# Kernel optimization log

Measured on AMD Instinct MI355X. Metric: run time of the kernel, lower is better.

The kernel has to match this reference:

```python
import jax, jax.numpy as jnp
import numpy as np

SHIFTS = [1, 2, 4]  # matches init_kwargs 'shifts' (all in range 0 < s < channels)


def setup_inputs() -> dict:
    key = jax.random.key(0)
    k1, k2, k3 = jax.random.split(key, 3)
    B, H, L, D = 4, 1, 2048, 512
    factor = 4
    proj_in = 2 * len(SHIFTS) * D  # cli_mode='full' -> 2 components per shift
    x = jax.random.normal(k1, (B, H, L, D), dtype=jnp.float32)
    W = jax.random.normal(k2, (factor, D), dtype=jnp.float32) * 0.05
    # glorot-ish scale for the projection kernel
    proj_kernel = jax.random.normal(k3, (proj_in, D), dtype=jnp.float32) * (1.0 / np.sqrt(proj_in))
    proj_bias = jnp.zeros((D,), dtype=jnp.float32)
    return {"x": x, "W": W, "proj_kernel": proj_kernel, "proj_bias": proj_bias}


def reference(x, W, proj_kernel, proj_bias):
    # x: (B, H, L, D); W: (k, D) slot multivectors
    k, D = W.shape
    B, H, L, _ = x.shape
    # coarse[-1] treated as zeros; non-anchor slots source previous coarse vector
    coarse_prev = jnp.pad(x, ((0, 0), (0, 0), (1, 0), (0, 0)))[:, :, :-1, :]
    # src: (B, H, L, k, D) — slots 0..k-2 from coarse_prev, slot k-1 (anchor) from x
    src = jnp.concatenate(
        [jnp.repeat(coarse_prev[:, :, :, None, :], k - 1, axis=3),
         x[:, :, :, None, :]],
        axis=3,
    )
    W_b = W[None, None, None, :, :]  # (1,1,1,k,D)
    components = []
    for s in SHIFTS:
        src_s = jnp.roll(src, s, axis=-1)
        W_s_b = jnp.roll(W, s, axis=-1)[None, None, None, :, :]
        sw = src * W_s_b
        components.append(sw - W_b * src_s)        # wedge part
        components.append(jax.nn.silu(sw))          # inner part (full mode)
    g = jnp.concatenate(components, axis=-1)  # (B,H,L,k, 2*len(shifts)*D)
    fine = jnp.einsum('bhlkc,cd->bhlkd', g, proj_kernel) + proj_bias
    return fine.reshape(B, H, L * k, D)
```

## Files before the change

### kernel.cpp

```cpp
#include <hip/hip_runtime.h>
#include <cstdint>
#include <cstddef>

#define D_DIM 512
#define L_DIM 2048
#define KB_DIM 2048
#define KS_DIM 1536
#define NROWS_X 2049
#define M_TOT 32768

typedef __bf16 bf16x8 __attribute__((ext_vector_type(8)));
typedef float  f32x4  __attribute__((ext_vector_type(4)));

__device__ __forceinline__ unsigned f2bf(float f) {
  unsigned u = __float_as_uint(f);
  u += 0x7FFF + ((u >> 16) & 1);
  return u >> 16;
}
__device__ __forceinline__ float bf2f(unsigned short u) {
  return __uint_as_float(((unsigned)u) << 16);
}
__device__ __forceinline__ void gld_lds16(const void* g, void* l) {
  __builtin_amdgcn_global_load_lds((const __attribute__((address_space(1))) void*)g,
                                   (__attribute__((address_space(3))) void*)l,
                                   16, 0, 0);
}

__global__ void convert_x(const float* __restrict__ x, unsigned short* __restrict__ XbfZ) {
  const int b = blockIdx.y;
  const int idx = blockIdx.x * 256 + threadIdx.x;
  if (idx >= NROWS_X * 128) return;
  const int rr = idx >> 7;
  const int c4 = idx & 127;
  uint2 p = {0u, 0u};
  if (rr > 0) {
    float4 v = reinterpret_cast<const float4*>(x)[((size_t)b * L_DIM + rr - 1) * 128 + c4];
    p.x = f2bf(v.x) | (f2bf(v.y) << 16);
    p.y = f2bf(v.z) | (f2bf(v.w) << 16);
  }
  reinterpret_cast<uint2*>(XbfZ)[((size_t)b * NROWS_X + rr) * 128 + c4] = p;
}

__global__ void build_B(const float* __restrict__ P, const float* __restrict__ W,
                        unsigned short* __restrict__ Ball,
                        unsigned short* __restrict__ Wtab, int buildWtab) {
  if (buildWtab && blockIdx.x == 0) {
    for (int i = threadIdx.x; i < 6144; i += 256) {
      const int c = i & 511; const int rest = i >> 9;
      const int si = rest % 3; const int jj = rest / 3;
      Wtab[(jj * 3 + si) * 512 + c] =
          (unsigned short)f2bf(W[jj * 512 + ((c - (1 << si)) & 511)]);
    }
  }
  const int bx = blockIdx.x;
  const int j = bx >> 6, dt = (bx >> 3) & 7, ct = bx & 7;
  const int t = threadIdx.x;
  const int d = dt * 64 + (t & 63);
  const int cbase = ct * 64 + (t >> 6) * 16;
  unsigned short bufd[16];
  unsigned short bufs[3][16];
  #pragma unroll
  for (int cc = 0; cc < 16; ++cc) {
    const int c = cbase + cc;
    float qd = 0.f;
    #pragma unroll
    for (int si = 0; si < 3; ++si) {
      const int s = 1 << si;
      const int cm = (c - s) & 511, cp = (c + s) & 511;
      qd += W[j * 512 + cm] * P[((size_t)(2 * si) * 512 + c) * 512 + d]
          - W[j * 512 + cp] * P[((size_t)(2 * si) * 512 + cp) * 512 + d];
      bufs[si][cc] = (unsigned short)f2bf(P[((size_t)(2 * si + 1) * 512 + c) * 512 + d]);
    }
    bufd[cc] = (unsigned short)f2bf(qd);
  }
  unsigned short* row = Ball + (size_t)(j * 512 + d) * KB_DIM;
  *reinterpret_cast<uint4*>(&row[cbase])     = *reinterpret_cast<uint4*>(&bufd[0]);
  *reinterpret_cast<uint4*>(&row[cbase + 8]) = *reinterpret_cast<uint4*>(&bufd[8]);
  #pragma unroll
  for (int si = 0; si < 3; ++si) {
    *reinterpret_cast<uint4*>(&row[512 + si * 512 + cbase])     = *reinterpret_cast<uint4*>(&bufs[si][0]);
    *reinterpret_cast<uint4*>(&row[512 + si * 512 + cbase + 8]) = *reinterpret_cast<uint4*>(&bufs[si][8]);
  }
}

__global__ void gs_gen(const unsigned short* __restrict__ XbfZ,
                       const unsigned short* __restrict__ Wtab,
                       unsigned short* __restrict__ GS) {
  const int m0 = blockIdx.x * 4;
  const int j = m0 >> 13, b = (m0 >> 11) & 3, lbase = m0 & 2047;
  const int r = threadIdx.x >> 6, lane = threadIdx.x & 63;
  const int l = lbase + r;
  const size_t vrow = (size_t)b * NROWS_X + l + (j == 3);
  union U { uint4 q; unsigned short s[8]; };
  U va;
  va.q = *reinterpret_cast<const uint4*>(XbfZ + vrow * 512 + lane * 8);
  unsigned short* o = GS + (size_t)(m0 + r) * KS_DIM + lane * 8;
  #pragma unroll
  for (int si = 0; si < 3; ++si) {
    U wa;
    wa.q = *reinterpret_cast<const uint4*>(Wtab + (j * 3 + si) * 512 + lane * 8);
    unsigned res[4];
    #pragma unroll
    for (int e = 0; e < 4; ++e) {
      float s0 = bf2f(va.s[2 * e])     * bf2f(wa.s[2 * e]);
      float s1 = bf2f(va.s[2 * e + 1]) * bf2f(wa.s[2 * e + 1]);
      float g0 = s0 * __builtin_amdgcn_rcpf(1.f + __expf(-s0));
      float g1 = s1 * __builtin_amdgcn_rcpf(1.f + __expf(-s1));
      res[e] = f2bf(g0) | (f2bf(g1) << 16);
    }
    uint4 ov = {res[0], res[1], res[2], res[3]};
    *reinterpret_cast<uint4*>(o + si * 512) = ov;
  }
}

__global__ __launch_bounds__(256) void gemm_main(
    const unsigned short* __restrict__ XbfZ, const unsigned short* __restrict__ GS,
    const unsigned short* __restrict__ Ball, const float* __restrict__ bias,
    float* __restrict__ out) {
  __shared__ alignas(16) unsigned short At[2][4096];
  __shared__ alignas(16) unsigned short Bt[2][4096];

  const int tid = threadIdx.x;
  const int bx = blockIdx.x;
  const int nt = bx >> 8;
  const int mt = bx & 255;
  const int j  = mt >> 6;
  const int b  = (mt >> 4) & 3;
  const int l0 = (mt & 15) * 128;
  const int n0 = nt * 128;

  const int rA = tid >> 2;
  const int qA = (tid & 3) ^ ((rA >> 2) & 3);
  const unsigned short* srcAd0 = XbfZ + (size_t)(b * NROWS_X + l0 + (j == 3) + rA) * 512 + qA * 8;
  const unsigned short* srcAd1 = srcAd0 + (size_t)64 * 512;
  const size_t mbase = (size_t)((j * 4 + b) * L_DIM + l0);
  const unsigned short* srcAs0 = GS + (mbase + rA) * KS_DIM + qA * 8;
  const unsigned short* srcAs1 = srcAs0 + (size_t)64 * KS_DIM;
  const unsigned short* srcB0 = Ball + (size_t)(j * 512 + n0 + rA) * KB_DIM + qA * 8;
  const unsigned short* srcB1 = srcB0 + (size_t)64 * KB_DIM;

  const int lane = tid & 63, wv = tid >> 6;
  const int wm = wv >> 1, wn = wv & 1;
  const int l16 = lane & 15, quad = lane >> 4;
  const int qf = quad ^ ((l16 >> 2) & 3);
  const int aBase = (wm * 64 + l16) * 32 + qf * 8;
  const int bBase = (wn * 64 + l16) * 32 + qf * 8;

  f32x4 acc[4][4];
  #pragma unroll
  for (int i = 0; i < 4; ++i)
    #pragma unroll
    for (int n = 0; n < 4; ++n)
      acc[i][n] = f32x4{0.f, 0.f, 0.f, 0.f};

  gld_lds16(srcAd0, &At[0][tid * 8]);
  gld_lds16(srcAd1, &At[0][(tid + 256) * 8]);
  gld_lds16(srcB0,  &Bt[0][tid * 8]);
  gld_lds16(srcB1,  &Bt[0][(tid + 256) * 8]);

  for (int it = 0; it < 64; ++it) {
    const int buf = it & 1;
    __syncthreads();
    if (it + 1 < 64) {
      const int nx = it + 1, nb = buf ^ 1;
      const unsigned short *a0, *a1;
      if (nx < 16) { a0 = srcAd0 + nx * 32; a1 = srcAd1 + nx * 32; }
      else { const int o = (nx - 16) * 32; a0 = srcAs0 + o; a1 = srcAs1 + o; }
      gld_lds16(a0, &At[nb][tid * 8]);
      gld_lds16(a1, &At[nb][(tid + 256) * 8]);
      gld_lds16(srcB0 + nx * 32, &Bt[nb][tid * 8]);
      gld_lds16(srcB1 + nx * 32, &Bt[nb][(tid + 256) * 8]);
    }
    bf16x8 af[4], bfr[4];
    #pragma unroll
    for (int mi = 0; mi < 4; ++mi) {
      uint4 rr = *reinterpret_cast<const uint4*>(&At[buf][aBase + mi * 512]);
      af[mi] = __builtin_bit_cast(bf16x8, rr);
    }
    #pragma unroll
    for (int ni = 0; ni < 4; ++ni) {
      uint4 rr = *reinterpret_cast<const uint4*>(&Bt[buf][bBase + ni * 512]);
      bfr[ni] = __builtin_bit_cast(bf16x8, rr);
    }
    #pragma unroll
    for (int mi = 0; mi < 4; ++mi)
      #pragma unroll
      for (int ni = 0; ni < 4; ++ni)
        acc[mi][ni] = __builtin_amdgcn_mfma_f32_16x16x32_bf16(af[mi], bfr[ni], acc[mi][ni], 0, 0, 0);
  }

  #pragma unroll
  for (int ni = 0; ni < 4; ++ni) {
    const int d = n0 + wn * 64 + ni * 16 + l16;
    const float bv = bias[d];
    #pragma unroll
    for (int mi = 0; mi < 4; ++mi) {
      const int lrow = l0 + wm * 64 + mi * 16 + quad * 4;
      #pragma unroll
      for (int rg = 0; rg < 4; ++rg) {
        out[((size_t)(b * L_DIM + lrow + rg) * 4 + j) * D_DIM + d] = acc[mi][ni][rg] + bv;
      }
    }
  }
}

__global__ __launch_bounds__(256, 2) void fused_gemm(
    const unsigned short* __restrict__ XbfZ, const unsigned short* __restrict__ Ball,
    const float* __restrict__ W, const float* __restrict__ bias,
    float* __restrict__ out) {
  __shared__ alignas(16) unsigned short Vt[2][4096];
  __shared__ alignas(16) unsigned short Bt[2][8192];
  __shared__ alignas(16) unsigned short At[128 * 40];
  __shared__ alignas(16) unsigned short Wr[3 * 512];

  const int tid = threadIdx.x;
  const int nt = blockIdx.x & 1;
  const int mt = blockIdx.x >> 1;
  const int j  = mt >> 6;
  const int b  = (mt >> 4) & 3;
  const int lt = mt & 15;
  const int l0 = lt * 128;
  const int n0 = nt * 256;
  const int base_l = l0 - ((j == 3) ? 0 : 1);

  #pragma unroll
  for (int i = 0; i < 6; ++i) {
    const int idx = tid + i * 256;
    const int si = idx >> 9, c = idx & 511, s = 1 << si;
    Wr[idx] = (unsigned short)f2bf(W[j * 512 + ((c - s) & 511)]);
  }

  const int lane = tid & 63, wv = tid >> 6;
  const int qv = (lane & 3) ^ ((lane >> 4) & 3);
  const int rsub = lane >> 2;
  const unsigned short* gA0 = XbfZ + ((size_t)(b * NROWS_X + 1 + base_l + (wv * 2) * 16 + rsub)) * 512 + qv * 8;
  const unsigned short* gA1 = gA0 + (size_t)16 * 512;
  const unsigned short* gB[4];
  #pragma unroll
  for (int pi = 0; pi < 4; ++pi)
    gB[pi] = Ball + (size_t)(j * 512 + n0 + (wv * 4 + pi) * 16 + rsub) * KB_DIM + qv * 8;
  const int vOff0 = wv * 1024 + lane * 8;
  const int bOff0 = wv * 2048 + lane * 8;

  const int am = tid >> 1;
  const int akh = (tid & 1) * 16;
  const int ch0 = (tid & 1) * 2;
  const int sswz = (am >> 2) & 3;
  unsigned short* aDst = &At[am * 40 + akh];

  const int l16 = lane & 15, quad = lane >> 4;
  const int wm = wv >> 1, wn = wv & 1;
  const int fsw = (l16 >> 2) & 3;
  const int aVoff = (wm * 64 + l16) * 32 + ((quad ^ fsw)) * 8;
  const int aSoff = (wm * 64 + l16) * 40 + quad * 8;
  const int bOffF = (wn * 128 + l16) * 32 + ((quad ^ fsw)) * 8;

  f32x4 acc[4][8];
  #pragma unroll
  for (int i = 0; i < 4; ++i)
    #pragma unroll
    for (int n = 0; n < 8; ++n)
      acc[i][n] = f32x4{0.f, 0.f, 0.f, 0.f};

  {
    gld_lds16(gA0, &Vt[0][vOff0]);
    gld_lds16(gA1, &Vt[0][vOff0 + 512]);
    #pragma unroll
    for (int pi = 0; pi < 4; ++pi)
      gld_lds16(gB[pi], &Bt[0][bOff0 + pi * 512]);
  }

  for (int it = 0; it < 64; ++it) {
    const int buf = it & 1;
    const int kk0 = it * 32;
    const int gi = kk0 >> 9;

    __syncthreads();

    if (it + 1 < 64) {
      const int nk = kk0 + 32;
      const int nv = nk & 511;
      gld_lds16(gA0 + nv, &Vt[buf ^ 1][vOff0]);
      gld_lds16(gA1 + nv, &Vt[buf ^ 1][vOff0 + 512]);
      #pragma unroll
      for (int pi = 0; pi < 4; ++pi)
        gld_lds16(gB[pi] + nk, &Bt[buf ^ 1][bOff0 + pi * 512]);
    }

    bf16x8 af[4], bfr[8];
    if (gi == 0) {
      #pragma unroll
      for (int mi = 0; mi < 4; ++mi) {
        uint4 r = *reinterpret_cast<const uint4*>(&Vt[buf][aVoff + mi * 512]);
        af[mi] = __builtin_bit_cast(bf16x8, r);
      }
    } else {
      const int si = gi - 1;
      const int ccbase = (kk0 & 511) + akh;
      uint4 v0 = *reinterpret_cast<const uint4*>(&Vt[buf][(am * 4 + ((ch0)     ^ sswz)) * 8]);
      uint4 v1 = *reinterpret_cast<const uint4*>(&Vt[buf][(am * 4 + ((ch0 + 1) ^ sswz)) * 8]);
      uint4 w0 = *reinterpret_cast<const uint4*>(&Wr[si * 512 + ccbase]);
      uint4 w1 = *reinterpret_cast<const uint4*>(&Wr[si * 512 + ccbase + 8]);
      union U { uint4 q[2]; unsigned short s[16]; };
      U va, wa; va.q[0] = v0; va.q[1] = v1; wa.q[0] = w0; wa.q[1] = w1;
      unsigned res[8];
      #pragma unroll
      for (int e = 0; e < 8; ++e) {
        float s0 = bf2f(va.s[2 * e])     * bf2f(wa.s[2 * e]);
        float s1 = bf2f(va.s[2 * e + 1]) * bf2f(wa.s[2 * e + 1]);
        float g0 = s0 * __builtin_amdgcn_rcpf(1.f + __expf(-s0));
        float g1 = s1 * __builtin_amdgcn_rcpf(1.f + __expf(-s1));
        res[e] = f2bf(g0) | (f2bf(g1) << 16);
      }
      uint4 o0 = {res[0], res[1], res[2], res[3]};
      uint4 o1 = {res[4], res[5], res[6], res[7]};
      *reinterpret_cast<uint4*>(aDst) = o0;
      *reinterpret_cast<uint4*>(aDst + 8) = o1;
      __syncthreads();
      #pragma unroll
      for (int mi = 0; mi < 4; ++mi) {
        uint4 r = *reinterpret_cast<const uint4*>(&At[aSoff + mi * 640]);
        af[mi] = __builtin_bit_cast(bf16x8, r);
      }
    }
    #pragma unroll
    for (int ni = 0; ni < 8; ++ni) {
      uint4 r = *reinterpret_cast<const uint4*>(&Bt[buf][bOffF + ni * 512]);
      bfr[ni] = __builtin_bit_cast(bf16x8, r);
    }
    #pragma unroll
    for (int mi = 0; mi < 4; ++mi)
      #pragma unroll
      for (int ni = 0; ni < 8; ++ni)
        acc[mi][ni] = __builtin_amdgcn_mfma_f32_16x16x32_bf16(af[mi], bfr[ni], acc[mi][ni], 0, 0, 0);
  }

  #pragma unroll
  for (int ni = 0; ni < 8; ++ni) {
    const int d = n0 + wn * 128 + ni * 16 + l16;
    const float bv = bias[d];
    #pragma unroll
    for (int mi = 0; mi < 4; ++mi) {
      const int lrow = l0 + wm * 64 + mi * 16 + quad * 4;
      #pragma unroll
      for (int rg = 0; rg < 4; ++rg) {
        out[((size_t)(b * L_DIM + lrow + rg) * 4 + j) * D_DIM + d] = acc[mi][ni][rg] + bv;
      }
    }
  }
}

extern "C" void kernel_launch(void* const* d_in, const int* in_sizes, int n_in,
                              void* d_out, int out_size, void* d_ws, size_t ws_size,
                              hipStream_t stream) {
  const float* x    = (const float*)d_in[0];
  const float* W    = (const float*)d_in[1];
  const float* P    = (const float*)d_in[2];
  const float* bias = (const float*)d_in[3];
  float* out = (float*)d_out;

  unsigned short* XbfZ = (unsigned short*)d_ws;
  unsigned short* Ball = XbfZ + (size_t)4 * NROWS_X * 512;
  unsigned short* Wtab = Ball + (size_t)4 * 512 * KB_DIM;
  unsigned short* GS   = Wtab + 6144;
  const size_t need_bytes =
      ((size_t)4 * NROWS_X * 512 + (size_t)4 * 512 * KB_DIM + 6144 +
       (size_t)M_TOT * KS_DIM) * 2;
  const bool primary = ws_size >= need_bytes;

  convert_x<<<dim3(1025, 4), 256, 0, stream>>>(x, XbfZ);
  build_B<<<256, 256, 0, stream>>>(P, W, Ball, Wtab, primary ? 1 : 0);
  if (primary) {
    gs_gen<<<8192, 256, 0, stream>>>(XbfZ, Wtab, GS);
    gemm_main<<<1024, 256, 0, stream>>>(XbfZ, GS, Ball, bias, out);
  } else {
    fused_gemm<<<512, 256, 0, stream>>>(XbfZ, Ball, W, bias, out);
  }
}
```

Measured before the change: 199.4 us.

## Load GEMM fragments directly from global into registers, removing LDS staging

The gemm_main kernel stops staging A and B tiles through double-buffered shared memory and instead has each wave load its MFMA fragments straight from global memory into registers, with an even/odd register double buffer to overlap loads with MFMAs. This removes LDS traffic and the per-iteration __syncthreads barriers. In exchange, tile data shared across waves is re-fetched from global/L2 (A by both wn waves, B by both wm waves), the per-lane 16-byte strided loads are less coalesced, and register pressure rises.

Measured after the change: 348.8 us. 74.9% more time.

```diff
diff --git a/kernel.cpp b/kernel.cpp
--- a/kernel.cpp
+++ b/kernel.cpp
@@ -117,9 +117,6 @@
     const unsigned short* __restrict__ XbfZ, const unsigned short* __restrict__ GS,
     const unsigned short* __restrict__ Ball, const float* __restrict__ bias,
     float* __restrict__ out) {
-  __shared__ alignas(16) unsigned short At[2][4096];
-  __shared__ alignas(16) unsigned short Bt[2][4096];
-
   const int tid = threadIdx.x;
   const int bx = blockIdx.x;
   const int nt = bx >> 8;
@@ -129,22 +126,26 @@
   const int l0 = (mt & 15) * 128;
   const int n0 = nt * 128;
 
-  const int rA = tid >> 2;
-  const int qA = (tid & 3) ^ ((rA >> 2) & 3);
-  const unsigned short* srcAd0 = XbfZ + (size_t)(b * NROWS_X + l0 + (j == 3) + rA) * 512 + qA * 8;
-  const unsigned short* srcAd1 = srcAd0 + (size_t)64 * 512;
-  const size_t mbase = (size_t)((j * 4 + b) * L_DIM + l0);
-  const unsigned short* srcAs0 = GS + (mbase + rA) * KS_DIM + qA * 8;
-  const unsigned short* srcAs1 = srcAs0 + (size_t)64 * KS_DIM;
-  const unsigned short* srcB0 = Ball + (size_t)(j * 512 + n0 + rA) * KB_DIM + qA * 8;
-  const unsigned short* srcB1 = srcB0 + (size_t)64 * KB_DIM;
-
   const int lane = tid & 63, wv = tid >> 6;
   const int wm = wv >> 1, wn = wv & 1;
   const int l16 = lane & 15, quad = lane >> 4;
-  const int qf = quad ^ ((l16 >> 2) & 3);
-  const int aBase = (wm * 64 + l16) * 32 + qf * 8;
-  const int bBase = (wn * 64 + l16) * 32 + qf * 8;
+
+  const unsigned short* pA[4];
+  {
+    const unsigned short* base =
+        XbfZ + ((size_t)b * NROWS_X + l0 + (j == 3) + wm * 64 + l16) * 512 + quad * 8;
+    #pragma unroll
+    for (int mi = 0; mi < 4; ++mi) pA[mi] = base + (size_t)mi * 16 * 512;
+  }
+  const unsigned short* pAg =
+      GS + ((size_t)((j * 4 + b) * L_DIM + l0 + wm * 64 + l16)) * KS_DIM + quad * 8;
+  const unsigned short* pB[4];
+  {
+    const unsigned short* base =
+        Ball + ((size_t)(j * 512 + n0 + wn * 64 + l16)) * KB_DIM + quad * 8;
+    #pragma unroll
+    for (int ni = 0; ni < 4; ++ni) pB[ni] = base + (size_t)ni * 16 * KB_DIM;
+  }
 
   f32x4 acc[4][4];
   #pragma unroll
@@ -153,41 +154,49 @@
     for (int n = 0; n < 4; ++n)
       acc[i][n] = f32x4{0.f, 0.f, 0.f, 0.f};
 
-  gld_lds16(srcAd0, &At[0][tid * 8]);
-  gld_lds16(srcAd1, &At[0][(tid + 256) * 8]);
-  gld_lds16(srcB0,  &Bt[0][tid * 8]);
-  gld_lds16(srcB1,  &Bt[0][(tid + 256) * 8]);
-
-  for (int it = 0; it < 64; ++it) {
-    const int buf = it & 1;
-    __syncthreads();
-    if (it + 1 < 64) {
-      const int nx = it + 1, nb = buf ^ 1;
-      const unsigned short *a0, *a1;
-      if (nx < 16) { a0 = srcAd0 + nx * 32; a1 = srcAd1 + nx * 32; }
-      else { const int o = (nx - 16) * 32; a0 = srcAs0 + o; a1 = srcAs1 + o; }
-      gld_lds16(a0, &At[nb][tid * 8]);
-      gld_lds16(a1, &At[nb][(tid + 256) * 8]);
-      gld_lds16(srcB0 + nx * 32, &Bt[nb][tid * 8]);
-      gld_lds16(srcB1 + nx * 32, &Bt[nb][(tid + 256) * 8]);
-    }
-    bf16x8 af[4], bfr[4];
-    #pragma unroll
-    for (int mi = 0; mi < 4; ++mi) {
-      uint4 rr = *reinterpret_cast<const uint4*>(&At[buf][aBase + mi * 512]);
-      af[mi] = __builtin_bit_cast(bf16x8, rr);
-    }
-    #pragma unroll
-    for (int ni = 0; ni < 4; ++ni) {
-      uint4 rr = *reinterpret_cast<const uint4*>(&Bt[buf][bBase + ni * 512]);
-      bfr[ni] = __builtin_bit_cast(bf16x8, rr);
-    }
-    #pragma unroll
-    for (int mi = 0; mi < 4; ++mi)
-      #pragma unroll
-      for (int ni = 0; ni < 4; ++ni)
-        acc[mi][ni] = __builtin_amdgcn_mfma_f32_16x16x32_bf16(af[mi], bfr[ni], acc[mi][ni], 0, 0, 0);
-  }
+  uint4 aE[4], bE[4], aO[4], bO[4];
+
+#define LOAD_SET(aset, bset)                                         \
+  do {                                                               \
+    _Pragma("unroll")                                                \
+    for (int mi = 0; mi < 4; ++mi) {                                 \
+      aset[mi] = *reinterpret_cast<const uint4*>(pA[mi]);            \
+      pA[mi] += 32;                                                  \
+    }                                                                \
+    _Pragma("unroll")                                                \
+    for (int ni = 0; ni < 4; ++ni) {                                 \
+      bset[ni] = *reinterpret_cast<const uint4*>(pB[ni]);            \
+      pB[ni] += 32;                                                  \
+    }                                                                \
+  } while (0)
+
+#define MFMA_SET(aset, bset)                                         \
+  do {                                                               \
+    _Pragma("unroll")                                                \
+    for (int mi = 0; mi < 4; ++mi) {                                 \
+      bf16x8 af = __builtin_bit_cast(bf16x8, aset[mi]);              \
+      _Pragma("unroll")                                              \
+      for (int ni = 0; ni < 4; ++ni) {                               \
+        bf16x8 bf = __builtin_bit_cast(bf16x8, bset[ni]);            \
+        acc[mi][ni] =                                                \
+            __builtin_amdgcn_mfma_f32_16x16x32_bf16(af, bf, acc[mi][ni], 0, 0, 0); \
+      }                                                              \
+    }                                                                \
+  } while (0)
+
+  LOAD_SET(aE, bE);
+  for (int h = 0; h < 32; ++h) {
+    LOAD_SET(aO, bO);
+    MFMA_SET(aE, bE);
+    if (h == 7) {
+      #pragma unroll
+      for (int mi = 0; mi < 4; ++mi) pA[mi] = pAg + (size_t)mi * 16 * KS_DIM;
+    }
+    if (h < 31) LOAD_SET(aE, bE);
+    MFMA_SET(aO, bO);
+  }
+#undef LOAD_SET
+#undef MFMA_SET
 
   #pragma unroll
   for (int ni = 0; ni < 4; ++ni) {
```
